# Kernel tuning notes

Measured on AMD Instinct MI355X. Metric: run time of the kernel, lower is better.

The kernel has to match this reference:

```python
import jax, jax.numpy as jnp
import numpy as np

B, L = 2, 2048
IN_DIM, HD_DIM, STATE_DIM = 512, 4096, 16
NUM_PATHS, ENT_DEPTH = 2, 2
ENT_STRENGTH, WALK_TIME = 0.3, 1.0


def _glorot(key, shape):
    lim = np.sqrt(6.0 / (shape[0] + shape[1]))
    return jax.random.uniform(key, shape, jnp.float32, -lim, lim)


def setup_inputs() -> dict:
    key = jax.random.key(0)
    ks = jax.random.split(key, 10)
    x = jax.random.normal(ks[0], (B, L, IN_DIM), jnp.float32)
    input_proj = _glorot(ks[1], (IN_DIM, HD_DIM))
    output_proj = _glorot(ks[2], (HD_DIM, IN_DIM))
    a_log = jax.random.uniform(ks[3], (STATE_DIM,), jnp.float32, -4.0, -1.0)
    b_proj = _glorot(ks[4], (HD_DIM, STATE_DIM))
    c_proj = _glorot(ks[5], (HD_DIM, STATE_DIM))
    dt_proj = jnp.full((HD_DIM,), 0.01, jnp.float32)
    skip_proj = jnp.ones((HD_DIM,), jnp.float32)  # diagonal skip, init 1.0
    amplitudes_real = jnp.full((NUM_PATHS,), 1.0 / np.sqrt(NUM_PATHS), jnp.float32)
    amplitudes_imag = 0.01 * jax.random.normal(ks[6], (NUM_PATHS,), jnp.float32)
    rotation_angles = jax.random.uniform(ks[7], (ENT_DEPTH, NUM_PATHS), jnp.float32, 0.0, 2.0 * np.pi)
    wh, _ = jnp.linalg.qr(jax.random.normal(ks[8], (NUM_PATHS, NUM_PATHS), jnp.float32))  # orthogonal init
    return dict(x=x, input_proj=input_proj, output_proj=output_proj, a_log=a_log,
                b_proj=b_proj, c_proj=c_proj, dt_proj=dt_proj, skip_proj=skip_proj,
                amplitudes_real=amplitudes_real, amplitudes_imag=amplitudes_imag,
                rotation_angles=rotation_angles, walk_hamiltonian=wh)


def _qhd_forward(x, input_proj, output_proj, a_log, b_proj, c_proj, dt_proj,
                 skip_proj, amp_r, amp_i, rot, walk_h):
    Bb, Ll, _ = x.shape
    K = amp_r.shape[0]
    dt = jax.nn.softplus(dt_proj)                                   # (D,)
    hd = jnp.einsum('bld,dh->blh', x, input_proj)                   # (B,L,D)
    # --- frequency-stratified superposition paths (K bands) ---
    Xf = jnp.fft.rfft(hd, axis=1)                                   # (B,F,D) complex
    F = Xf.shape[1]
    band = jnp.clip(jnp.arange(F) * K // F, 0, K - 1)
    masks = (band[None, :] == jnp.arange(K)[:, None]).astype(hd.dtype)  # (K,F)
    x_paths = jnp.fft.irfft(Xf[None] * masks[:, None, :, None], n=Ll, axis=2)  # (K,B,L,D)
    # --- FFT-domain diagonal selective SSM (causal conv with exp decay) ---
    a = -jnp.exp(a_log)                                             # (N,)
    dt_bar = jnp.mean(dt)
    t_idx = jnp.arange(Ll, dtype=hd.dtype)
    decay = jnp.exp(a[None, :] * dt_bar * t_idx[:, None])           # (L,N)
    Bt = jnp.einsum('kbld,dn->kbln', x_paths * dt, b_proj)          # (K,B,L,N)
    n2 = 2 * Ll
    h = jnp.fft.irfft(jnp.fft.rfft(Bt, n=n2, axis=2) * jnp.fft.rfft(decay, n=n2, axis=0),
                      n=n2, axis=2)[:, :, :Ll, :]                   # (K,B,L,N)
    y_paths = jnp.einsum('kbln,dn->kbld', h, c_proj)                # (K,B,L,D)
    # --- VQC entanglement (RY-style phase + quantum-walk mixing) ---
    alpha = amp_r.astype(jnp.complex64) + 1j * amp_i.astype(jnp.complex64)
    A = 1j * (ENT_STRENGTH * WALK_TIME) * walk_h.astype(jnp.complex64)
    U = jnp.eye(K, dtype=jnp.complex64) + A + (A @ A) / 2.0 + (A @ A @ A) / 6.0
    for d in range(rot.shape[0]):
        alpha = jnp.exp(1j * rot[d].astype(jnp.complex64)) * alpha
        alpha = U @ alpha
    # --- Born rule collapse ---
    w = jnp.abs(alpha) ** 2
    w = (w / jnp.sum(w)).astype(hd.dtype)                           # (K,)
    y = jnp.einsum('k,kbld->bld', w, y_paths) + hd * skip_proj      # diagonal skip
    return jnp.einsum('blh,hd->bld', y, output_proj)                # (B,L,in_dim)


def reference(x, input_proj, output_proj, a_log, b_proj, c_proj, dt_proj,
              skip_proj, amplitudes_real, amplitudes_imag, rotation_angles,
              walk_hamiltonian):
    return _qhd_forward(x, input_proj, output_proj, a_log, b_proj, c_proj,
                        dt_proj, skip_proj, amplitudes_real, amplitudes_imag,
                        rotation_angles, walk_hamiltonian)
```

## Files before the change

kernel.cpp:

```cpp
#include <hip/hip_runtime.h>
#include <cstdint>

typedef unsigned short ushort_t;
typedef __bf16 bf16x8 __attribute__((ext_vector_type(8)));
typedef float f32x4 __attribute__((ext_vector_type(4)));

#define PI_F 3.14159265358979323846f

__device__ __forceinline__ ushort_t f2bf(float f) {
  uint32_t x = __float_as_uint(f);
  x += 0x7fffu + ((x >> 16) & 1u);
  return (ushort_t)(x >> 16);
}
__device__ __forceinline__ float bf2f(ushort_t u) {
  return __uint_as_float(((uint32_t)u) << 16);
}
__device__ __forceinline__ float softplusf(float x) {
  return (x > 20.f) ? x : log1pf(expf(x));
}
__device__ __forceinline__ void async_ld16(ushort_t* lds, const ushort_t* g) {
  __builtin_amdgcn_global_load_lds(
      (const __attribute__((address_space(1))) uint32_t*)g,
      (__attribute__((address_space(3))) uint32_t*)lds, 16, 0, 0);
}
__device__ __forceinline__ void load16f(const float* p, float* v) {
  const float4* q = reinterpret_cast<const float4*>(p);
  float4 t0 = q[0], t1 = q[1], t2 = q[2], t3 = q[3];
  v[0]=t0.x; v[1]=t0.y; v[2]=t0.z; v[3]=t0.w;
  v[4]=t1.x; v[5]=t1.y; v[6]=t1.z; v[7]=t1.w;
  v[8]=t2.x; v[9]=t2.y; v[10]=t2.z; v[11]=t2.w;
  v[12]=t3.x; v[13]=t3.y; v[14]=t3.z; v[15]=t3.w;
}


__global__ __launch_bounds__(256) void cast_bf16(const float* __restrict__ in,
                                                 ushort_t* __restrict__ out, int n) {
  int i = blockIdx.x * 256 + threadIdx.x;
  if (i < n) out[i] = f2bf(in[i]);
}

__global__ __launch_bounds__(256) void transpose_cast(const float* __restrict__ in,
                                                      ushort_t* __restrict__ out,
                                                      int R, int C) {
  __shared__ float t[32][33];
  int bc = blockIdx.x * 32;
  int br = blockIdx.y * 32;
  int tx = threadIdx.x, ty = threadIdx.y;
#pragma unroll
  for (int i = ty; i < 32; i += 8)
    t[i][tx] = in[(size_t)(br + i) * C + bc + tx];
  __syncthreads();
#pragma unroll
  for (int i = ty; i < 32; i += 8)
    out[(size_t)(bc + i) * R + br + tx] = f2bf(t[tx][i]);
}

__global__ __launch_bounds__(256) void bdt_kernel(const float* __restrict__ bp,
                                                  const float* __restrict__ dtp,
                                                  float* __restrict__ bdt) {
  int i = blockIdx.x * 256 + threadIdx.x;
  bdt[i] = bp[i] * softplusf(dtp[i >> 4]);
}

__global__ __launch_bounds__(256) void small_setup(const float* __restrict__ dtp,
                                                   const float* __restrict__ a_log,
                                                   const float* __restrict__ ar,
                                                   const float* __restrict__ ai,
                                                   const float* __restrict__ rot,
                                                   const float* __restrict__ wh,
                                                   float* __restrict__ sc) {
  __shared__ float red[256];
  float s = 0.f;
  for (int i = threadIdx.x; i < 4096; i += 256) s += softplusf(dtp[i]);
  red[threadIdx.x] = s;
  __syncthreads();
  for (int st = 128; st > 0; st >>= 1) {
    if (threadIdx.x < st) red[threadIdx.x] += red[threadIdx.x + st];
    __syncthreads();
  }
  if (threadIdx.x == 0) {
    float dtbar = red[0] / 4096.f;
    float B00 = 0.3f * wh[0], B01 = 0.3f * wh[1], B10 = 0.3f * wh[2], B11 = 0.3f * wh[3];
    float C00 = B00*B00 + B01*B10, C01 = B00*B01 + B01*B11;
    float C10 = B10*B00 + B11*B10, C11 = B10*B01 + B11*B11;
    float D00 = C00*B00 + C01*B10, D01 = C00*B01 + C01*B11;
    float D10 = C10*B00 + C11*B10, D11 = C10*B01 + C11*B11;
    float Ur00 = 1.f - 0.5f*C00, Ur01 = -0.5f*C01, Ur10 = -0.5f*C10, Ur11 = 1.f - 0.5f*C11;
    float Ui00 = B00 - D00/6.f, Ui01 = B01 - D01/6.f, Ui10 = B10 - D10/6.f, Ui11 = B11 - D11/6.f;
    float a0r = ar[0], a0i = ai[0], a1r = ar[1], a1i = ai[1];
#pragma unroll
    for (int d = 0; d < 2; ++d) {
      float c0 = cosf(rot[d*2+0]), s0 = sinf(rot[d*2+0]);
      float c1 = cosf(rot[d*2+1]), s1 = sinf(rot[d*2+1]);
      float t0r = a0r*c0 - a0i*s0, t0i = a0r*s0 + a0i*c0;
      float t1r = a1r*c1 - a1i*s1, t1i = a1r*s1 + a1i*c1;
      a0r = Ur00*t0r - Ui00*t0i + Ur01*t1r - Ui01*t1i;
      a0i = Ur00*t0i + Ui00*t0r + Ur01*t1i + Ui01*t1r;
      a1r = Ur10*t0r - Ui10*t0i + Ur11*t1r - Ui11*t1i;
      a1i = Ur10*t0i + Ui10*t0r + Ur11*t1i + Ui11*t1r;
    }
    float p0 = a0r*a0r + a0i*a0i, p1 = a1r*a1r + a1i*a1i;
    float inv = 1.f / (p0 + p1);
    sc[0] = p0 * inv; sc[1] = p1 * inv; sc[2] = dtbar;
#pragma unroll
    for (int n = 0; n < 16; ++n) {
      float a = -expf(a_log[n]);
      sc[8 + n]  = expf(a * dtbar);
      sc[24 + n] = expf(a * dtbar * 32.f);
    }
  }
}


template<int BM, int BN, int WR, int WC, bool OBF>
__global__ __launch_bounds__(256)
void gemm_bf16(const ushort_t* __restrict__ A, const ushort_t* __restrict__ Bt,
               void* __restrict__ Cv, int M, int N, int Kc, int lda, int ldb, int swz) {
  constexpr int BK = 64;
  constexpr int WMR = BM / WR;
  constexpr int WNC = BN / WC;
  constexpr int MI = WMR / 16;
  constexpr int NI = WNC / 16;
  constexpr int NCA = BM * BK * 2 / 1024;
  constexpr int NCB = BN * BK * 2 / 1024;

  __shared__ ushort_t lA[BM * BK];
  __shared__ ushort_t lB[BN * BK];

  const int tid = threadIdx.x;
  const int w = tid >> 6, lane = tid & 63;
  const int wr = w / WC, wc = w % WC;
  const int r = lane & 15, g = lane >> 4;

  const int nbx = gridDim.x;
  int bid = blockIdx.y * nbx + blockIdx.x;
  if (swz) {
    const int nwg = nbx * gridDim.y;
    bid = (bid & 7) * (nwg >> 3) + (bid >> 3);
  }
  const int m0 = (bid / nbx) * BM, n0 = (bid % nbx) * BN;
  const int kz = blockIdx.z * Kc;

  f32x4 acc[MI][NI];
#pragma unroll
  for (int mi = 0; mi < MI; ++mi)
#pragma unroll
    for (int ni = 0; ni < NI; ++ni)
      acc[mi][ni] = (f32x4){0.f, 0.f, 0.f, 0.f};

  const int ktiles = Kc >> 6;
  for (int kt = 0; kt < ktiles; ++kt) {
    const int k0 = kz + (kt << 6);
    for (int c = w; c < NCA; c += 4) {
      int byteoff = (c << 10) + (lane << 4);
      int row = byteoff >> 7;
      int scol = (byteoff & 127) ^ ((row & 7) << 4);
      async_ld16(&lA[c << 9], &A[(size_t)(m0 + row) * lda + k0 + (scol >> 1)]);
    }
    for (int c = w; c < NCB; c += 4) {
      int byteoff = (c << 10) + (lane << 4);
      int row = byteoff >> 7;
      int scol = (byteoff & 127) ^ ((row & 7) << 4);
      async_ld16(&lB[c << 9], &Bt[(size_t)(n0 + row) * ldb + k0 + (scol >> 1)]);
    }
    __syncthreads();
#pragma unroll
    for (int kk = 0; kk < 2; ++kk) {
      bf16x8 av[MI], bv[NI];
#pragma unroll
      for (int mi = 0; mi < MI; ++mi) {
        int row = wr * WMR + mi * 16 + r;
        int off = (((kk << 2) + g) ^ (row & 7)) << 3;
        av[mi] = *reinterpret_cast<const bf16x8*>(&lA[row * 64 + off]);
      }
#pragma unroll
      for (int ni = 0; ni < NI; ++ni) {
        int row = wc * WNC + ni * 16 + r;
        int off = (((kk << 2) + g) ^ (row & 7)) << 3;
        bv[ni] = *reinterpret_cast<const bf16x8*>(&lB[row * 64 + off]);
      }
#pragma unroll
      for (int mi = 0; mi < MI; ++mi)
#pragma unroll
        for (int ni = 0; ni < NI; ++ni)
          acc[mi][ni] = __builtin_amdgcn_mfma_f32_16x16x32_bf16(av[mi], bv[ni], acc[mi][ni], 0, 0, 0);
    }
    __syncthreads();
  }
  const size_t zoff = (size_t)blockIdx.z * (size_t)M * (size_t)N;
#pragma unroll
  for (int mi = 0; mi < MI; ++mi)
#pragma unroll
    for (int ni = 0; ni < NI; ++ni) {
      int row = m0 + wr * WMR + mi * 16 + g * 4;
      int col = n0 + wc * WNC + ni * 16 + r;
#pragma unroll
      for (int j = 0; j < 4; ++j) {
        size_t idx = zoff + (size_t)(row + j) * N + col;
        if (OBF) ((ushort_t*)Cv)[idx] = f2bf(acc[mi][ni][j]);
        else     ((float*)Cv)[idx]   = acc[mi][ni][j];
      }
    }
}


__global__ __launch_bounds__(256)
void reduceK(const float4* __restrict__ p, float4* __restrict__ out) {
  int i = blockIdx.x * 256 + threadIdx.x;
  float4 a = p[i];
  float4 b = p[i + 524288];
  float4 c = p[i + 1048576];
  float4 d = p[i + 1572864];
  float4 o;
  o.x = a.x + b.x + c.x + d.x;
  o.y = a.y + b.y + c.y + d.y;
  o.z = a.z + b.z + c.z + d.z;
  o.w = a.w + b.w + c.w + d.w;
  out[i] = o;
}


__global__ __launch_bounds__(256)
void bhd_kernel(const ushort_t* __restrict__ hd, const float* __restrict__ bdt,
                float* __restrict__ Bhd) {
  const int m0 = blockIdx.x << 2;
  const int tid = threadIdx.x;
  float acc[4][16];
#pragma unroll
  for (int a = 0; a < 4; ++a)
#pragma unroll
    for (int n = 0; n < 16; ++n) acc[a][n] = 0.f;

  for (int d = tid; d < 4096; d += 256) {
    float bv[16];
    load16f(bdt + (d << 4), bv);
    float hv[4];
#pragma unroll
    for (int a = 0; a < 4; ++a) hv[a] = bf2f(hd[(size_t)(m0 + a) * 4096 + d]);
#pragma unroll
    for (int a = 0; a < 4; ++a)
#pragma unroll
      for (int n = 0; n < 16; ++n) acc[a][n] += hv[a] * bv[n];
  }
  __shared__ float sred[4][4][16];
  const int w = tid >> 6, lane = tid & 63;
#pragma unroll
  for (int a = 0; a < 4; ++a)
#pragma unroll
    for (int n = 0; n < 16; ++n) {
      float v = acc[a][n];
#pragma unroll
      for (int off2 = 32; off2 > 0; off2 >>= 1) v += __shfl_down(v, off2);
      if (lane == 0) sred[w][a][n] = v;
    }
  __syncthreads();
  if (tid < 64) {
    int a = tid >> 4, n = tid & 15;
    Bhd[(size_t)(m0 + a) * 16 + n] =
        sred[0][a][n] + sred[1][a][n] + sred[2][a][n] + sred[3][a][n];
  }
}


__global__ __launch_bounds__(256)
void freq_ssm(const float* __restrict__ Bhd, const float* __restrict__ sc,
              float* __restrict__ h) {
  const int blk = blockIdx.x;
  const int b = blk >> 4, n = blk & 15;
  const int tid = threadIdx.x;
  __shared__ float2 X[2048];
  __shared__ float carr[64], pre[64];
  const float w0 = sc[0], w1 = sc[1];
  const float r = sc[8 + n], r32 = sc[24 + n];

  for (int l = tid; l < 2048; l += 256) {
    X[l].x = Bhd[(size_t)(b * 2048 + l) * 16 + n];
    X[l].y = 0.f;
  }
  for (int ls = 10; ls >= 0; --ls) {
    int s = 1 << ls;
    __syncthreads();
    for (int q = tid; q < 1024; q += 256) {
      int j = q & (s - 1);
      int base = (q >> ls) << (ls + 1);
      int i0 = base + j, i1 = i0 + s;
      float2 a = X[i0], bb = X[i1];
      X[i0].x = a.x + bb.x; X[i0].y = a.y + bb.y;
      float tx = a.x - bb.x, ty = a.y - bb.y;
      float ang = -PI_F * (float)j / (float)s;
      float sn, cs; sincosf(ang, &sn, &cs);
      X[i1].x = tx * cs - ty * sn;
      X[i1].y = tx * sn + ty * cs;
    }
  }
  __syncthreads();
  for (int i = tid; i < 2048; i += 256) {
    unsigned f = __brev((unsigned)i) >> 21;
    float wv = (f <= 512u || f >= 1536u) ? w0 : w1;
    X[i].x *= wv; X[i].y *= wv;
  }
  for (int ls = 0; ls <= 10; ++ls) {
    int s = 1 << ls;
    __syncthreads();
    for (int q = tid; q < 1024; q += 256) {
      int j = q & (s - 1);
      int base = (q >> ls) << (ls + 1);
      int i0 = base + j, i1 = i0 + s;
      float ang = PI_F * (float)j / (float)s;
      float sn, cs; sincosf(ang, &sn, &cs);
      float2 bb = X[i1];
      float bx = bb.x * cs - bb.y * sn;
      float by = bb.x * sn + bb.y * cs;
      float2 a = X[i0];
      X[i0].x = a.x + bx; X[i0].y = a.y + by;
      X[i1].x = a.x - bx; X[i1].y = a.y - by;
    }
  }
  __syncthreads();
  const float inv = 1.0f / 2048.0f;
  if (tid < 64) {
    float c = 0.f;
    int base = tid * 32;
#pragma unroll
    for (int i = 0; i < 32; ++i) c = r * c + X[base + i].x * inv;
    carr[tid] = c;
  }
  __syncthreads();
  if (tid == 0) {
    float s = 0.f;
    for (int j2 = 0; j2 < 64; ++j2) { pre[j2] = s; s = s * r32 + carr[j2]; }
  }
  __syncthreads();
  if (tid < 64) {
    float s = pre[tid];
    int base = tid * 32;
#pragma unroll
    for (int i = 0; i < 32; ++i) {
      s = r * s + X[base + i].x * inv;
      h[(size_t)(b * 2048 + base + i) * 16 + n] = s;
    }
  }
}


__global__ __launch_bounds__(256)
void y_kernel(const ushort_t* __restrict__ hd, const float* __restrict__ hv,
              const float* __restrict__ c_proj, const float* __restrict__ skip,
              ushort_t* __restrict__ y) {
  const int m0 = blockIdx.x << 2;
  const int tid = threadIdx.x;
  __shared__ float sh[4][16];
  if (tid < 64) sh[tid >> 4][tid & 15] = hv[(size_t)(m0 + (tid >> 4)) * 16 + (tid & 15)];
  __syncthreads();
  float hreg[4][16];
#pragma unroll
  for (int a = 0; a < 4; ++a)
#pragma unroll
    for (int n = 0; n < 16; ++n) hreg[a][n] = sh[a][n];

  for (int d = tid; d < 4096; d += 256) {
    float cv[16];
    load16f(c_proj + (d << 4), cv);
    float sk = skip[d];
#pragma unroll
    for (int a = 0; a < 4; ++a) {
      float acc = bf2f(hd[(size_t)(m0 + a) * 4096 + d]) * sk;
#pragma unroll
      for (int n = 0; n < 16; ++n) acc += cv[n] * hreg[a][n];
      y[(size_t)(m0 + a) * 4096 + d] = f2bf(acc);
    }
  }
}


extern "C" void kernel_launch(void* const* d_in, const int* in_sizes, int n_in,
                              void* d_out, int out_size, void* d_ws, size_t ws_size,
                              hipStream_t stream) {
  (void)in_sizes; (void)n_in; (void)out_size; (void)ws_size;
  const float* x      = (const float*)d_in[0];
  const float* Win    = (const float*)d_in[1];
  const float* Wout   = (const float*)d_in[2];
  const float* a_log  = (const float*)d_in[3];
  const float* b_proj = (const float*)d_in[4];
  const float* c_proj = (const float*)d_in[5];
  const float* dt_proj= (const float*)d_in[6];
  const float* skip   = (const float*)d_in[7];
  const float* ampr   = (const float*)d_in[8];
  const float* ampi   = (const float*)d_in[9];
  const float* rot    = (const float*)d_in[10];
  const float* wh     = (const float*)d_in[11];
  float* out = (float*)d_out;

  char* ws = (char*)d_ws;
  ushort_t* A1  = (ushort_t*)(ws + 0);
  ushort_t* Wt1 = (ushort_t*)(ws + 4194304);
  ushort_t* Wt2 = (ushort_t*)(ws + 8388608);
  float*    bdt = (float*)(ws + 12582912);
  float*    Bhd = (float*)(ws + 12845056);
  float*    hv  = (float*)(ws + 13107200);
  float*    sc  = (float*)(ws + 13369344);
  ushort_t* hd  = (ushort_t*)(ws + 13369600);
  float*    part= (float*)(ws + 13369600);
  ushort_t* y   = (ushort_t*)(ws + 46924032);

  cast_bf16<<<8192, 256, 0, stream>>>(x, A1, 4096 * 512);
  transpose_cast<<<dim3(128, 16), dim3(32, 8), 0, stream>>>(Win, Wt1, 512, 4096);
  transpose_cast<<<dim3(16, 128), dim3(32, 8), 0, stream>>>(Wout, Wt2, 4096, 512);
  bdt_kernel<<<256, 256, 0, stream>>>(b_proj, dt_proj, bdt);
  small_setup<<<1, 256, 0, stream>>>(dt_proj, a_log, ampr, ampi, rot, wh, sc);

  gemm_bf16<128, 128, 2, 2, true><<<dim3(32, 32), 256, 0, stream>>>(
      A1, Wt1, hd, 4096, 4096, 512, 512, 512, 1);
  bhd_kernel<<<1024, 256, 0, stream>>>(hd, bdt, Bhd);
  freq_ssm<<<32, 256, 0, stream>>>(Bhd, sc, hv);
  y_kernel<<<1024, 256, 0, stream>>>(hd, hv, c_proj, skip, y);
  gemm_bf16<64, 128, 1, 4, false><<<dim3(4, 64, 4), 256, 0, stream>>>(
      y, Wt2, part, 4096, 512, 1024, 4096, 4096, 1);
  reduceK<<<2048, 256, 0, stream>>>((const float4*)part, (float4*)out);
}
```

Baseline: 277.2 us.

## Vectorize hd loads in bhd_kernel and retile y_kernel for c_proj register reuse

bhd_kernel now has each thread load 8 contiguous bf16 hd values with one 16-byte load per row, instead of one strided scalar load per element. y_kernel moves to a 2D grid: each thread holds c_proj rows for two adjacent d columns in registers and loops over 64 rows of m, with the h vectors shared through LDS. The intent is to stop re-reading c_proj once per 4-row block and to use wider, coalesced hd and y accesses. The trade-off is more registers per thread and fewer, longer-running blocks.

```diff
diff --git a/kernel.cpp b/kernel.cpp
--- a/kernel.cpp
+++ b/kernel.cpp
@@ -231,16 +231,29 @@
 #pragma unroll
     for (int n = 0; n < 16; ++n) acc[a][n] = 0.f;
 
-  for (int d = tid; d < 4096; d += 256) {
-    float bv[16];
-    load16f(bdt + (d << 4), bv);
-    float hv[4];
-#pragma unroll
-    for (int a = 0; a < 4; ++a) hv[a] = bf2f(hd[(size_t)(m0 + a) * 4096 + d]);
-#pragma unroll
-    for (int a = 0; a < 4; ++a)
-#pragma unroll
-      for (int n = 0; n < 16; ++n) acc[a][n] += hv[a] * bv[n];
+#pragma unroll
+  for (int it = 0; it < 2; ++it) {
+    const int d = (it * 256 + tid) << 3;
+    float hf[4][8];
+#pragma unroll
+    for (int a = 0; a < 4; ++a) {
+      uint4 pk = *reinterpret_cast<const uint4*>(&hd[(size_t)(m0 + a) * 4096 + d]);
+      const uint32_t* pw = (const uint32_t*)&pk;
+#pragma unroll
+      for (int j = 0; j < 4; ++j) {
+        hf[a][2*j]   = bf2f((ushort_t)(pw[j] & 0xffff));
+        hf[a][2*j+1] = bf2f((ushort_t)(pw[j] >> 16));
+      }
+    }
+#pragma unroll
+    for (int j = 0; j < 8; ++j) {
+      float bv[16];
+      load16f(bdt + ((size_t)(d + j) << 4), bv);
+#pragma unroll
+      for (int a = 0; a < 4; ++a)
+#pragma unroll
+        for (int n = 0; n < 16; ++n) acc[a][n] += hf[a][j] * bv[n];
+    }
   }
   __shared__ float sred[4][4][16];
   const int w = tid >> 6, lane = tid & 63;
@@ -347,28 +360,34 @@
 void y_kernel(const ushort_t* __restrict__ hd, const float* __restrict__ hv,
               const float* __restrict__ c_proj, const float* __restrict__ skip,
               ushort_t* __restrict__ y) {
-  const int m0 = blockIdx.x << 2;
   const int tid = threadIdx.x;
-  __shared__ float sh[4][16];
-  if (tid < 64) sh[tid >> 4][tid & 15] = hv[(size_t)(m0 + (tid >> 4)) * 16 + (tid & 15)];
-  __syncthreads();
-  float hreg[4][16];
-#pragma unroll
-  for (int a = 0; a < 4; ++a)
-#pragma unroll
-    for (int n = 0; n < 16; ++n) hreg[a][n] = sh[a][n];
-
-  for (int d = tid; d < 4096; d += 256) {
-    float cv[16];
-    load16f(c_proj + (d << 4), cv);
-    float sk = skip[d];
-#pragma unroll
-    for (int a = 0; a < 4; ++a) {
-      float acc = bf2f(hd[(size_t)(m0 + a) * 4096 + d]) * sk;
-#pragma unroll
-      for (int n = 0; n < 16; ++n) acc += cv[n] * hreg[a][n];
-      y[(size_t)(m0 + a) * 4096 + d] = f2bf(acc);
-    }
+  const int d0 = blockIdx.x * 512 + tid * 2;
+  const int m0 = blockIdx.y * 64;
+  __shared__ float hsh[64][16];
+  reinterpret_cast<float4*>(&hsh[0][0])[tid] =
+      reinterpret_cast<const float4*>(hv + (size_t)m0 * 16)[tid];
+
+  float c0[16], c1[16];
+  load16f(c_proj + (size_t)d0 * 16, c0);
+  load16f(c_proj + (size_t)(d0 + 1) * 16, c1);
+  const float sk0 = skip[d0], sk1 = skip[d0 + 1];
+  __syncthreads();
+
+#pragma unroll 4
+  for (int m = 0; m < 64; ++m) {
+    const size_t base = (size_t)(m0 + m) * 4096 + d0;
+    uint32_t pair = *reinterpret_cast<const uint32_t*>(&hd[base]);
+    float a0 = bf2f((ushort_t)(pair & 0xffffu)) * sk0;
+    float a1 = bf2f((ushort_t)(pair >> 16)) * sk1;
+    const float4* hm = reinterpret_cast<const float4*>(hsh[m]);
+#pragma unroll
+    for (int q = 0; q < 4; ++q) {
+      float4 hq = hm[q];
+      a0 += c0[4*q+0] * hq.x + c0[4*q+1] * hq.y + c0[4*q+2] * hq.z + c0[4*q+3] * hq.w;
+      a1 += c1[4*q+0] * hq.x + c1[4*q+1] * hq.y + c1[4*q+2] * hq.z + c1[4*q+3] * hq.w;
+    }
+    uint32_t o = (uint32_t)f2bf(a0) | ((uint32_t)f2bf(a1) << 16);
+    *reinterpret_cast<uint32_t*>(&y[base]) = o;
   }
 }
 
@@ -413,7 +432,7 @@
       A1, Wt1, hd, 4096, 4096, 512, 512, 512, 1);
   bhd_kernel<<<1024, 256, 0, stream>>>(hd, bdt, Bhd);
   freq_ssm<<<32, 256, 0, stream>>>(Bhd, sc, hv);
-  y_kernel<<<1024, 256, 0, stream>>>(hd, hv, c_proj, skip, y);
+  y_kernel<<<dim3(8, 64), 256, 0, stream>>>(hd, hv, c_proj, skip, y);
   gemm_bf16<64, 128, 1, 4, false><<<dim3(4, 64, 4), 256, 0, stream>>>(
       y, Wt2, part, 4096, 512, 1024, 4096, 4096, 1);
   reduceK<<<2048, 256, 0, stream>>>((const float4*)part, (float4*)out);
```

Result: slower. 322.3 us (+16.3%).

## Reassociate B projection through input weights and fuse y epilogue into first GEMM

Applied to the files above, without the earlier changes.

Computes Bhd as x·(Win·bdt) using two skinny matvec-style kernels, so the B projection no longer needs the materialized hd tensor. The first GEMM's epilogue then directly produces y = hd*skip + C·h, removing both the hd bf16 write/readback and the separate bhd and y kernels. The trade-off is a heavier GEMM epilogue that loads c_proj and h rows, plus fp32 reassociation that changes rounding relative to the bf16 hd path.

```diff
diff --git a/kernel.cpp b/kernel.cpp
--- a/kernel.cpp
+++ b/kernel.cpp
@@ -112,10 +112,54 @@
 }
 
 
-template<int BM, int BN, int WR, int WC, bool OBF>
+__global__ __launch_bounds__(256)
+void skinny16(const float* __restrict__ A, const float* __restrict__ Bm,
+              float* __restrict__ C, int K, int lda) {
+  const int m0 = blockIdx.x << 2;
+  const int tid = threadIdx.x;
+  float acc[4][16];
+#pragma unroll
+  for (int a = 0; a < 4; ++a)
+#pragma unroll
+    for (int n = 0; n < 16; ++n) acc[a][n] = 0.f;
+
+  for (int d = tid; d < K; d += 256) {
+    float bv[16];
+    load16f(Bm + (size_t)d * 16, bv);
+    float av[4];
+#pragma unroll
+    for (int a = 0; a < 4; ++a) av[a] = A[(size_t)(m0 + a) * lda + d];
+#pragma unroll
+    for (int a = 0; a < 4; ++a)
+#pragma unroll
+      for (int n = 0; n < 16; ++n) acc[a][n] += av[a] * bv[n];
+  }
+  __shared__ float sred[4][4][16];
+  const int w = tid >> 6, lane = tid & 63;
+#pragma unroll
+  for (int a = 0; a < 4; ++a)
+#pragma unroll
+    for (int n = 0; n < 16; ++n) {
+      float v = acc[a][n];
+#pragma unroll
+      for (int off2 = 32; off2 > 0; off2 >>= 1) v += __shfl_down(v, off2);
+      if (lane == 0) sred[w][a][n] = v;
+    }
+  __syncthreads();
+  if (tid < 64) {
+    int a = tid >> 4, n = tid & 15;
+    C[(size_t)(m0 + a) * 16 + n] =
+        sred[0][a][n] + sred[1][a][n] + sred[2][a][n] + sred[3][a][n];
+  }
+}
+
+
+template<int BM, int BN, int WR, int WC, bool OBF, bool FUSE>
 __global__ __launch_bounds__(256)
 void gemm_bf16(const ushort_t* __restrict__ A, const ushort_t* __restrict__ Bt,
-               void* __restrict__ Cv, int M, int N, int Kc, int lda, int ldb, int swz) {
+               void* __restrict__ Cv, int M, int N, int Kc, int lda, int ldb, int swz,
+               const float* __restrict__ hvp, const float* __restrict__ cj,
+               const float* __restrict__ skp) {
   constexpr int BK = 64;
   constexpr int WMR = BM / WR;
   constexpr int WNC = BN / WC;
@@ -187,20 +231,55 @@
     }
     __syncthreads();
   }
-  const size_t zoff = (size_t)blockIdx.z * (size_t)M * (size_t)N;
-#pragma unroll
-  for (int mi = 0; mi < MI; ++mi)
+
+  if constexpr (FUSE) {
+    float* hsh = reinterpret_cast<float*>(lA);
+    {
+      const float4* src = reinterpret_cast<const float4*>(hvp + (size_t)m0 * 16);
+      float4* dst = reinterpret_cast<float4*>(hsh);
+      for (int q = tid; q < BM * 4; q += 256) dst[q] = src[q];
+    }
+    float cr[NI][16];
+    float skv[NI];
+    int colg[NI];
 #pragma unroll
     for (int ni = 0; ni < NI; ++ni) {
-      int row = m0 + wr * WMR + mi * 16 + g * 4;
-      int col = n0 + wc * WNC + ni * 16 + r;
+      colg[ni] = n0 + wc * WNC + ni * 16 + r;
+      load16f(cj + (size_t)colg[ni] * 16, cr[ni]);
+      skv[ni] = skp[colg[ni]];
+    }
+    __syncthreads();
+#pragma unroll
+    for (int mi = 0; mi < MI; ++mi)
 #pragma unroll
       for (int j = 0; j < 4; ++j) {
-        size_t idx = zoff + (size_t)(row + j) * N + col;
-        if (OBF) ((ushort_t*)Cv)[idx] = f2bf(acc[mi][ni][j]);
-        else     ((float*)Cv)[idx]   = acc[mi][ni][j];
+        int row_l = wr * WMR + mi * 16 + g * 4 + j;
+        float hr[16];
+        load16f(hsh + row_l * 16, hr);
+#pragma unroll
+        for (int ni = 0; ni < NI; ++ni) {
+          float v = acc[mi][ni][j] * skv[ni];
+#pragma unroll
+          for (int n = 0; n < 16; ++n) v += cr[ni][n] * hr[n];
+          ((ushort_t*)Cv)[(size_t)(m0 + row_l) * N + colg[ni]] = f2bf(v);
+        }
       }
-    }
+  } else {
+    const size_t zoff = (size_t)blockIdx.z * (size_t)M * (size_t)N;
+#pragma unroll
+    for (int mi = 0; mi < MI; ++mi)
+#pragma unroll
+      for (int ni = 0; ni < NI; ++ni) {
+        int row = m0 + wr * WMR + mi * 16 + g * 4;
+        int col = n0 + wc * WNC + ni * 16 + r;
+#pragma unroll
+        for (int j = 0; j < 4; ++j) {
+          size_t idx = zoff + (size_t)(row + j) * N + col;
+          if (OBF) ((ushort_t*)Cv)[idx] = f2bf(acc[mi][ni][j]);
+          else     ((float*)Cv)[idx]   = acc[mi][ni][j];
+        }
+      }
+  }
 }
 
 
@@ -221,48 +300,6 @@
 
 
 __global__ __launch_bounds__(256)
-void bhd_kernel(const ushort_t* __restrict__ hd, const float* __restrict__ bdt,
-                float* __restrict__ Bhd) {
-  const int m0 = blockIdx.x << 2;
-  const int tid = threadIdx.x;
-  float acc[4][16];
-#pragma unroll
-  for (int a = 0; a < 4; ++a)
-#pragma unroll
-    for (int n = 0; n < 16; ++n) acc[a][n] = 0.f;
-
-  for (int d = tid; d < 4096; d += 256) {
-    float bv[16];
-    load16f(bdt + (d << 4), bv);
-    float hv[4];
-#pragma unroll
-    for (int a = 0; a < 4; ++a) hv[a] = bf2f(hd[(size_t)(m0 + a) * 4096 + d]);
-#pragma unroll
-    for (int a = 0; a < 4; ++a)
-#pragma unroll
-      for (int n = 0; n < 16; ++n) acc[a][n] += hv[a] * bv[n];
-  }
-  __shared__ float sred[4][4][16];
-  const int w = tid >> 6, lane = tid & 63;
-#pragma unroll
-  for (int a = 0; a < 4; ++a)
-#pragma unroll
-    for (int n = 0; n < 16; ++n) {
-      float v = acc[a][n];
-#pragma unroll
-      for (int off2 = 32; off2 > 0; off2 >>= 1) v += __shfl_down(v, off2);
-      if (lane == 0) sred[w][a][n] = v;
-    }
-  __syncthreads();
-  if (tid < 64) {
-    int a = tid >> 4, n = tid & 15;
-    Bhd[(size_t)(m0 + a) * 16 + n] =
-        sred[0][a][n] + sred[1][a][n] + sred[2][a][n] + sred[3][a][n];
-  }
-}
-
-
-__global__ __launch_bounds__(256)
 void freq_ssm(const float* __restrict__ Bhd, const float* __restrict__ sc,
               float* __restrict__ h) {
   const int blk = blockIdx.x;
@@ -338,36 +375,6 @@
     for (int i = 0; i < 32; ++i) {
       s = r * s + X[base + i].x * inv;
       h[(size_t)(b * 2048 + base + i) * 16 + n] = s;
-    }
-  }
-}
-
-
-__global__ __launch_bounds__(256)
-void y_kernel(const ushort_t* __restrict__ hd, const float* __restrict__ hv,
-              const float* __restrict__ c_proj, const float* __restrict__ skip,
-              ushort_t* __restrict__ y) {
-  const int m0 = blockIdx.x << 2;
-  const int tid = threadIdx.x;
-  __shared__ float sh[4][16];
-  if (tid < 64) sh[tid >> 4][tid & 15] = hv[(size_t)(m0 + (tid >> 4)) * 16 + (tid & 15)];
-  __syncthreads();
-  float hreg[4][16];
-#pragma unroll
-  for (int a = 0; a < 4; ++a)
-#pragma unroll
-    for (int n = 0; n < 16; ++n) hreg[a][n] = sh[a][n];
-
-  for (int d = tid; d < 4096; d += 256) {
-    float cv[16];
-    load16f(c_proj + (d << 4), cv);
-    float sk = skip[d];
-#pragma unroll
-    for (int a = 0; a < 4; ++a) {
-      float acc = bf2f(hd[(size_t)(m0 + a) * 4096 + d]) * sk;
-#pragma unroll
-      for (int n = 0; n < 16; ++n) acc += cv[n] * hreg[a][n];
-      y[(size_t)(m0 + a) * 4096 + d] = f2bf(acc);
     }
   }
 }
@@ -396,12 +403,12 @@
   ushort_t* Wt1 = (ushort_t*)(ws + 4194304);
   ushort_t* Wt2 = (ushort_t*)(ws + 8388608);
   float*    bdt = (float*)(ws + 12582912);
-  float*    Bhd = (float*)(ws + 12845056);
-  float*    hv  = (float*)(ws + 13107200);
-  float*    sc  = (float*)(ws + 13369344);
-  ushort_t* hd  = (ushort_t*)(ws + 13369600);
-  float*    part= (float*)(ws + 13369600);
-  ushort_t* y   = (ushort_t*)(ws + 46924032);
+  float*    Wb  = (float*)(ws + 12845056);
+  float*    Bhd = (float*)(ws + 12910592);
+  float*    hv  = (float*)(ws + 13172736);
+  float*    sc  = (float*)(ws + 13434880);
+  ushort_t* y   = (ushort_t*)(ws + 13435136);
+  float*    part= (float*)(ws + 46989568);
 
   cast_bf16<<<8192, 256, 0, stream>>>(x, A1, 4096 * 512);
   transpose_cast<<<dim3(128, 16), dim3(32, 8), 0, stream>>>(Win, Wt1, 512, 4096);
@@ -409,12 +416,14 @@
   bdt_kernel<<<256, 256, 0, stream>>>(b_proj, dt_proj, bdt);
   small_setup<<<1, 256, 0, stream>>>(dt_proj, a_log, ampr, ampi, rot, wh, sc);
 
-  gemm_bf16<128, 128, 2, 2, true><<<dim3(32, 32), 256, 0, stream>>>(
-      A1, Wt1, hd, 4096, 4096, 512, 512, 512, 1);
-  bhd_kernel<<<1024, 256, 0, stream>>>(hd, bdt, Bhd);
+  skinny16<<<128, 256, 0, stream>>>(Win, bdt, Wb, 4096, 4096);
+  skinny16<<<1024, 256, 0, stream>>>(x, Wb, Bhd, 512, 512);
   freq_ssm<<<32, 256, 0, stream>>>(Bhd, sc, hv);
-  y_kernel<<<1024, 256, 0, stream>>>(hd, hv, c_proj, skip, y);
-  gemm_bf16<64, 128, 1, 4, false><<<dim3(4, 64, 4), 256, 0, stream>>>(
-      y, Wt2, part, 4096, 512, 1024, 4096, 4096, 1);
+
+  gemm_bf16<128, 128, 2, 2, true, true><<<dim3(32, 32), 256, 0, stream>>>(
+      A1, Wt1, y, 4096, 4096, 512, 512, 512, 1, hv, c_proj, skip);
+
+  gemm_bf16<64, 128, 1, 4, false, false><<<dim3(4, 64, 4), 256, 0, stream>>>(
+      y, Wt2, part, 4096, 512, 1024, 4096, 4096, 1, nullptr, nullptr, nullptr);
   reduceK<<<2048, 256, 0, stream>>>((const float4*)part, (float4*)out);
 }
```

Measured after the change: 253.7 us. -8.5%, faster.
